# Optimization experiments

Hardware: AMD Instinct MI355X
Metric: run time of the kernel (lower is better)

The kernel has to match this reference:

```python
import jax, jax.numpy as jnp
import numpy as np

SAMPLERATE = 22050
N_OCTAVES = 16
N_SAMPLES = 32768
MIN_FREQ = 20.0 / (SAMPLERATE // 2)
MAX_FREQ = 3000.0 / (SAMPLERATE // 2)
FREQ_RANGE = MAX_FREQ - MIN_FREQ
BASE_RESONANCE = 0.01


def max_norm(x, axis=-1, eps=1e-8):
    return x / (jnp.max(jnp.abs(x), axis=axis, keepdims=True) + eps)


def exponential_decay(decay_values, n_octaves):
    # decay_values: (B, E, 1). Note the original applies sigmoid here on top of
    # the sigmoid already applied in forward (sigmoid_decay=True) -> double sigmoid.
    dv = jax.nn.sigmoid(decay_values)  # (B, E, 1)
    resonance_factor = (1.0 - BASE_RESONANCE) * 0.99
    decay = BASE_RESONANCE + dv * resonance_factor  # (B, E, 1)
    logd = jnp.log(decay + 1e-12)
    b, e, _ = decay_values.shape
    # cumsum of a per-(b,e) constant over octaves, then exp (matches torch code;
    # F.interpolate to size==n_octaves is the identity here)
    logd = jnp.broadcast_to(logd, (b, e, n_octaves))
    return jnp.exp(jnp.cumsum(logd, axis=-1))  # (B, E, O)


def setup_inputs() -> dict:
    key = jax.random.key(0)
    k1, k2, k3 = jax.random.split(key, 3)
    B, E = 8, 64
    return {
        "f0": jax.random.uniform(k1, (B, E, 1), dtype=jnp.float32),
        "decay_coefficients": jax.random.normal(k2, (B, E, 1), dtype=jnp.float32),
        "unused": jnp.zeros((B, E, 1), dtype=jnp.float32),
        "freq_spacing": jax.random.uniform(k3, (B, E, 1), dtype=jnp.float32),
    }


def reference(f0, decay_coefficients, unused, freq_spacing):
    b, e, _ = f0.shape
    O, S = N_OCTAVES, N_SAMPLES

    f0 = jnp.abs(f0)  # (B, E, 1)
    # sigmoid_decay=True path: sigmoid applied before exponential_decay
    exp_decays = exponential_decay(jax.nn.sigmoid(decay_coefficients), O)  # (B, E, O)

    f0 = (MIN_FREQ + f0 * FREQ_RANGE) * jnp.pi  # (B, E, 1)

    # freq_spacing repeated over octaves then cumsum -> per-octave factors
    factors = jnp.cumsum(jnp.broadcast_to(freq_spacing, (b, e, O)), axis=-1)
    f0s = f0 * factors  # (B, E, O)

    # nyquist cutoff
    f0s = f0s * (f0s < 1.0)

    # phase: cumsum over samples of constant per-octave frequency (faithful to torch)
    phase = jnp.cumsum(jnp.broadcast_to(f0s[..., None], (b, e, O, S)), axis=-1)
    osc = jnp.sin(phase)  # (B, E, O, S)

    osc = osc * exp_decays[..., None]
    osc = jnp.sum(osc, axis=2)  # (B, E, S)
    return max_norm(osc, axis=-1)
```

## Files before the change

kernel.cpp:

```cpp
#include <hip/hip_runtime.h>
#include <math.h>

#define N_OCT 16
#define NS    32768
#define TPB   512
#define SPT   (NS / TPB)
#define N_BE  512

__global__ __launch_bounds__(TPB, 1)
void f0res_kernel(const float* __restrict__ f0_in,
                  const float* __restrict__ dc_in,
                  const float* __restrict__ fs_in,
                  float* __restrict__ out)
{
    extern __shared__ float smem[];
    __shared__ float wmax[TPB / 64];

    const int be = blockIdx.x;
    const int t  = threadIdx.x;

    const float f0a = fabsf(f0_in[be]);
    const float dc  = dc_in[be];
    const float fs  = fs_in[be];

    const float MINF = (float)(20.0 / 11025.0);
    const float FRNG = (float)(3000.0 / 11025.0 - 20.0 / 11025.0);

    const float s1    = 1.0f / (1.0f + __expf(-dc));
    const float dv    = 1.0f / (1.0f + __expf(-s1));
    const float decay = 0.01f + dv * 0.9801f;
    const float logd  = __logf(decay + 1e-12f);
    const float f0r   = (MINF + f0a * FRNG) * 3.14159274101257324f;

    float sv[N_OCT], cv[N_OCT], cd[N_OCT], sd[N_OCT], amp[N_OCT];
    float cl = 0.f, cf = 0.f;
    const double inv2pi = 0.15915494309189535;
    #pragma unroll
    for (int o = 0; o < N_OCT; ++o) {
        cl += logd;
        cf += fs;
        float ed  = __expf(cl);
        float f0s = f0r * cf;
        float a   = ed;
        if (!(f0s < 1.0f)) { a = 0.0f; f0s = 0.0f; }
        amp[o] = a;
        double r  = (double)f0s * inv2pi;
        double p0 = r * (double)(t + 1);
        p0 -= floor(p0);
        sv[o] = __builtin_amdgcn_sinf((float)p0);
        cv[o] = __builtin_amdgcn_cosf((float)p0);
        double st = r * (double)TPB;
        st -= floor(st);
        sd[o] = __builtin_amdgcn_sinf((float)st);
        cd[o] = __builtin_amdgcn_cosf((float)st);
    }

    float lmax = 0.0f;
    #pragma unroll 4
    for (int k = 0; k < SPT; ++k) {
        float acc = 0.0f;
        #pragma unroll
        for (int o = 0; o < N_OCT; ++o) {
            acc = fmaf(amp[o], sv[o], acc);
            float ns = fmaf(sv[o], cd[o],  cv[o] * sd[o]);
            float nc = fmaf(cv[o], cd[o], -(sv[o] * sd[o]));
            sv[o] = ns;
            cv[o] = nc;
        }
        smem[k * TPB + t] = acc;
        lmax = fmaxf(lmax, fabsf(acc));
    }

    #pragma unroll
    for (int off = 32; off > 0; off >>= 1)
        lmax = fmaxf(lmax, __shfl_down(lmax, off, 64));
    if ((t & 63) == 0) wmax[t >> 6] = lmax;
    __syncthreads();
    float bmax = wmax[0];
    #pragma unroll
    for (int w = 1; w < TPB / 64; ++w) bmax = fmaxf(bmax, wmax[w]);

    const float norm = 1.0f / (bmax + 1e-8f);
    float4*       out4 = (float4*)(out + (size_t)be * NS);
    const float4* s4   = (const float4*)smem;
    #pragma unroll
    for (int j = 0; j < NS / 4 / TPB; ++j) {
        int i = j * TPB + t;
        float4 v = s4[i];
        v.x *= norm; v.y *= norm; v.z *= norm; v.w *= norm;
        out4[i] = v;
    }
}

extern "C" void kernel_launch(void* const* d_in, const int* in_sizes, int n_in,
                              void* d_out, int out_size, void* d_ws, size_t ws_size,
                              hipStream_t stream) {
    const float* f0 = (const float*)d_in[0];
    const float* dc = (const float*)d_in[1];
    const float* fs = (const float*)d_in[3];
    float* out = (float*)d_out;
    hipLaunchKernelGGL(f0res_kernel, dim3(N_BE), dim3(TPB),
                       NS * sizeof(float), stream, f0, dc, fs, out);
}
```

Before: 110.0 us.

## Switch oscillator to Chebyshev two-term recurrence with packed FMA and 1024 threads

Replaces the per-octave sin/cos rotation update with a second-order Chebyshev recurrence x_{n+1} = 2cos(d)·x_n − x_{n-1}. The 2cos coefficient is split into a high and a low float part to limit error growth over the recurrence steps. Octave pairs are packed into float2 vectors so the compiler can emit packed FMA instructions, which cuts the FLOPs per sample. The block size doubles to 1024 threads, halving samples per thread. This risks extra accumulated rounding error from the recurrence and heavier per-thread setup that now uses double-precision cos.

```diff
diff --git a/kernel.cpp b/kernel.cpp
--- a/kernel.cpp
+++ b/kernel.cpp
@@ -2,12 +2,19 @@
 #include <math.h>
 
 #define N_OCT 16
+#define NPAIR 8
 #define NS    32768
-#define TPB   512
+#define TPB   1024
 #define SPT   (NS / TPB)
 #define N_BE  512
 
-__global__ __launch_bounds__(TPB, 1)
+typedef float v2f __attribute__((ext_vector_type(2)));
+
+static __device__ __forceinline__ v2f fma2(v2f a, v2f b, v2f c) {
+    return __builtin_elementwise_fma(a, b, c);
+}
+
+__global__ __launch_bounds__(TPB)
 void f0res_kernel(const float* __restrict__ f0_in,
                   const float* __restrict__ dc_in,
                   const float* __restrict__ fs_in,
@@ -32,7 +39,8 @@
     const float logd  = __logf(decay + 1e-12f);
     const float f0r   = (MINF + f0a * FRNG) * 3.14159274101257324f;
 
-    float sv[N_OCT], cv[N_OCT], cd[N_OCT], sd[N_OCT], amp[N_OCT];
+    v2f xp[NPAIR], xc[NPAIR], c2h[NPAIR], c2l[NPAIR], amp2[NPAIR];
+
     float cl = 0.f, cf = 0.f;
     const double inv2pi = 0.15915494309189535;
     #pragma unroll
@@ -43,30 +51,43 @@
         float f0s = f0r * cf;
         float a   = ed;
         if (!(f0s < 1.0f)) { a = 0.0f; f0s = 0.0f; }
-        amp[o] = a;
+
         double r  = (double)f0s * inv2pi;
         double p0 = r * (double)(t + 1);
         p0 -= floor(p0);
-        sv[o] = __builtin_amdgcn_sinf((float)p0);
-        cv[o] = __builtin_amdgcn_cosf((float)p0);
-        double st = r * (double)TPB;
-        st -= floor(st);
-        sd[o] = __builtin_amdgcn_sinf((float)st);
-        cd[o] = __builtin_amdgcn_cosf((float)st);
+        double pm = r * (double)(t + 1 - TPB);
+        pm -= floor(pm);
+        float xcur  = __builtin_amdgcn_sinf((float)p0);
+        float xprev = __builtin_amdgcn_sinf((float)pm);
+
+        double drev = r * (double)TPB;
+        drev -= floor(drev);
+        double c2d = 2.0 * cos(drev * 6.283185307179586);
+        float  ch  = (float)c2d;
+        float  clo = (float)(c2d - (double)ch);
+
+        const int j = o >> 1, q = o & 1;
+        if (q == 0) {
+            xc[j].x = xcur;  xp[j].x = xprev;
+            c2h[j].x = ch;   c2l[j].x = clo;  amp2[j].x = a;
+        } else {
+            xc[j].y = xcur;  xp[j].y = xprev;
+            c2h[j].y = ch;   c2l[j].y = clo;  amp2[j].y = a;
+        }
     }
 
     float lmax = 0.0f;
     #pragma unroll 4
     for (int k = 0; k < SPT; ++k) {
-        float acc = 0.0f;
+        v2f acc2 = (v2f)(0.0f);
         #pragma unroll
-        for (int o = 0; o < N_OCT; ++o) {
-            acc = fmaf(amp[o], sv[o], acc);
-            float ns = fmaf(sv[o], cd[o],  cv[o] * sd[o]);
-            float nc = fmaf(cv[o], cd[o], -(sv[o] * sd[o]));
-            sv[o] = ns;
-            cv[o] = nc;
+        for (int j = 0; j < NPAIR; ++j) {
+            acc2 = fma2(amp2[j], xc[j], acc2);
+            v2f xn = fma2(c2h[j], xc[j], fma2(c2l[j], xc[j], -xp[j]));
+            xp[j] = xc[j];
+            xc[j] = xn;
         }
+        float acc = acc2.x + acc2.y;
         smem[k * TPB + t] = acc;
         lmax = fmaxf(lmax, fabsf(acc));
     }
```

Measured after the change: 129.6 us. +17.9%, slower.
